# Kernel optimization log

Measured on AMD Instinct MI355X. Metric: run time of the kernel, lower is better.

Reference implementation:

```python
import jax, jax.numpy as jnp
import numpy as np

B, N, D = 8, 2048, 1024
DC = 1024          # d_center
K = 4              # num_centers
NUM_JUMPS = 2
SPAN = 2
FIN = (2 + 2 * NUM_JUMPS + 1) * D  # 7*D

def _gelu(x):
    return jax.nn.gelu(x, approximate=False)  # torch nn.GELU default is exact erf

def setup_inputs() -> dict:
    key = jax.random.key(0)
    ks = jax.random.split(key, 16)
    s = lambda k, *sh: jax.random.normal(k, sh, dtype=jnp.float32) * 0.02
    return {
        "queries": jax.random.normal(ks[0], (B, N, D), dtype=jnp.float32),
        "fr_w1": s(ks[1], FIN, D), "fr_b1": jnp.zeros((D,), jnp.float32),
        "fr_w2": s(ks[2], D, D),   "fr_b2": jnp.zeros((D,), jnp.float32),
        "tc_w1": s(ks[3], D, DC),  "tc_b1": jnp.zeros((DC,), jnp.float32),
        "tc_w2": s(ks[4], DC, DC), "tc_b2": jnp.zeros((DC,), jnp.float32),
        "centers": jax.random.normal(ks[5], (K, DC), dtype=jnp.float32),
        "fc_w1": s(ks[6], D + DC, D), "fc_b1": jnp.zeros((D,), jnp.float32),
        "fc_w2": s(ks[7], D, D),      "fc_b2": jnp.zeros((D,), jnp.float32),
        "g_w": s(ks[8], D + DC, D),   "g_b": jnp.zeros((D,), jnp.float32),
    }

def reference(queries, fr_w1, fr_b1, fr_w2, fr_b2,
              tc_w1, tc_b1, tc_w2, tc_b2, centers,
              fc_w1, fc_b1, fc_w2, fc_b2, g_w, g_b):
    x = queries
    shifts = [1, -1, 0]  # left, right, x
    for i in range(1, NUM_JUMPS + 1):
        shifts += [i * SPAN, -i * SPAN]
    fusion = jnp.concatenate([jnp.roll(x, s, axis=1) for s in shifts], axis=-1)  # [B,N,7D]
    x_ring = _gelu(fusion @ fr_w1 + fr_b1) @ fr_w2 + fr_b2                       # [B,N,D]
    token_proj = _gelu(x_ring @ tc_w1 + tc_b1) @ tc_w2 + tc_b2                   # [B,N,DC]
    w = jax.nn.softmax(jnp.einsum('bnd,kd->bnk', token_proj, centers), axis=-1)  # [B,N,K]
    weighted = jnp.einsum('bnk,kd->bnd', w, centers)                             # [B,N,DC]
    fus2 = jnp.concatenate([x_ring, weighted], axis=-1)                          # [B,N,D+DC]
    gate = jax.nn.sigmoid(fus2 @ g_w + g_b)
    fc = _gelu(fus2 @ fc_w1 + fc_b1) @ fc_w2 + fc_b2
    return gate * fc + (1.0 - gate) * x_ring
```

## Files before the change

kernel.cpp:

```cpp
#include <hip/hip_runtime.h>
#include <hip/hip_bf16.h>
#include <math.h>

typedef unsigned short u16;
typedef __attribute__((ext_vector_type(8))) short short8;
typedef __attribute__((ext_vector_type(4))) float f32x4;


__device__ __forceinline__ float bf2f(u16 b) {
  return __uint_as_float(((unsigned int)b) << 16);
}
__device__ __forceinline__ u16 f2bf(float f) {
  unsigned int u = __float_as_uint(f);
  u += 0x7FFFu + ((u >> 16) & 1u);
  return (u16)(u >> 16);
}
__device__ __forceinline__ float gelu_exact(float x) {
  return 0.5f * x * (1.0f + erff(x * 0.70710678118654752f));
}

__device__ __forceinline__ void cp16(const void* g, void* l) {
  __builtin_amdgcn_global_load_lds(
      (const __attribute__((address_space(1))) unsigned int*)g,
      (__attribute__((address_space(3))) unsigned int*)l, 16, 0, 0);
}

template <int MODE, bool GATHER>
__global__ __launch_bounds__(256) void gemm128(
    const u16* __restrict__ A, int lda, const u16* __restrict__ Wt, int K,
    const float* __restrict__ bias, const float* __restrict__ bias2,
    void* __restrict__ out0, int ldo0, void* __restrict__ out1,
    const float* __restrict__ gate, const float* __restrict__ xring) {
  __shared__ __align__(16) u16 As[128 * 64];
  __shared__ __align__(16) u16 Bs[128 * 64];

  const int tid = threadIdx.x;
  const int lane = tid & 63;
  const int wave = tid >> 6;
  const int wm = wave >> 1;
  const int wn = wave & 1;

  const unsigned linear = blockIdx.y * gridDim.x + blockIdx.x;
  const unsigned xcd = linear & 7u;
  const unsigned pos = linear >> 3;
  const unsigned bx = pos % gridDim.x;
  const unsigned by = xcd * (gridDim.y >> 3) + pos / gridDim.x;
  const int m0 = by * 128;
  const int n0 = bx * 128;

  const int srow = lane >> 3;
  const int sq = lane & 7;
  const int sqs = sq ^ srow;

  f32x4 acc[4][4];
#pragma unroll
  for (int i = 0; i < 4; i++)
#pragma unroll
    for (int j = 0; j < 4; j++) acc[i][j] = (f32x4){0.f, 0.f, 0.f, 0.f};

  for (int k0 = 0; k0 < K; k0 += 64) {
#pragma unroll
    for (int i = 0; i < 4; i++) {
      const int rloc = wave * 32 + i * 8 + srow;
      long gofs;
      if (GATHER) {
        const int seg = k0 >> 10;
        int shift;
        switch (seg) {
          case 0: shift = 1; break;
          case 1: shift = -1; break;
          case 2: shift = 0; break;
          case 3: shift = 2; break;
          case 4: shift = -2; break;
          case 5: shift = 4; break;
          default: shift = -4; break;
        }
        const int m = m0 + rloc;
        const int b = m >> 11;
        const int nsrc = ((m & 2047) - shift) & 2047;
        gofs = (long)((b << 11) | nsrc) * 1024 + (k0 & 1023) + sqs * 8;
      } else {
        gofs = (long)(m0 + rloc) * lda + k0 + sqs * 8;
      }
      cp16(A + gofs, &As[(wave * 32 + i * 8) * 64]);
    }
#pragma unroll
    for (int i = 0; i < 4; i++) {
      const int rloc = wave * 32 + i * 8 + srow;
      const long gofs = (long)(n0 + rloc) * K + k0 + sqs * 8;
      cp16(Wt + gofs, &Bs[(wave * 32 + i * 8) * 64]);
    }
    __syncthreads();

    const int q4 = lane >> 4;
    const int r16 = lane & 15;
#pragma unroll
    for (int kk = 0; kk < 2; kk++) {
      short8 af[4], bf[4];
#pragma unroll
      for (int mi = 0; mi < 4; mi++) {
        const int row = wm * 64 + mi * 16 + r16;
        const int q = (kk * 4 + q4) ^ (row & 7);
        af[mi] = *(const short8*)&As[row * 64 + q * 8];
      }
#pragma unroll
      for (int ni = 0; ni < 4; ni++) {
        const int row = wn * 64 + ni * 16 + r16;
        const int q = (kk * 4 + q4) ^ (row & 7);
        bf[ni] = *(const short8*)&Bs[row * 64 + q * 8];
      }
#pragma unroll
      for (int mi = 0; mi < 4; mi++)
#pragma unroll
        for (int ni = 0; ni < 4; ni++)
          acc[mi][ni] = __builtin_amdgcn_mfma_f32_16x16x32_bf16(
              af[mi], bf[ni], acc[mi][ni], 0, 0, 0);
    }
    __syncthreads();
  }

  const int ccol = lane & 15;
  const int crow = (lane >> 4) * 4;
#pragma unroll
  for (int mi = 0; mi < 4; mi++) {
#pragma unroll
    for (int ni = 0; ni < 4; ni++) {
#pragma unroll
      for (int r = 0; r < 4; r++) {
        const int m = m0 + wm * 64 + mi * 16 + crow + r;
        const int n = n0 + wn * 64 + ni * 16 + ccol;
        if (MODE == 5) {
          if (n < 1024) {
            const float v = acc[mi][ni][r] + bias[n];
            ((float*)out0)[(long)m * 1024 + n] = 1.0f / (1.0f + expf(-v));
          } else {
            const float v = acc[mi][ni][r] + bias2[n - 1024];
            ((u16*)out1)[(long)m * 1024 + (n - 1024)] = f2bf(gelu_exact(v));
          }
        } else {
          const float v = acc[mi][ni][r] + bias[n];
          if (MODE == 0) {
            ((u16*)out0)[(long)m * ldo0 + n] = f2bf(gelu_exact(v));
          } else if (MODE == 1) {
            ((float*)out1)[(long)m * 1024 + n] = v;
            ((u16*)out0)[(long)m * ldo0 + n] = f2bf(v);
          } else if (MODE == 2) {
            ((u16*)out0)[(long)m * ldo0 + n] = f2bf(v);
          } else {
            const float g = gate[(long)m * 1024 + n];
            const float xr = xring[(long)m * 1024 + n];
            ((float*)out0)[(long)m * ldo0 + n] = g * v + (1.0f - g) * xr;
          }
        }
      }
    }
  }
}

__global__ __launch_bounds__(256) void cast_bf16(const float* __restrict__ in,
                                                 u16* __restrict__ out, int n4) {
  const long i = (long)blockIdx.x * 256 + threadIdx.x;
  if (i < n4) {
    const float4 v = ((const float4*)in)[i];
    ushort4 o;
    o.x = f2bf(v.x); o.y = f2bf(v.y); o.z = f2bf(v.z); o.w = f2bf(v.w);
    ((ushort4*)out)[i] = o;
  }
}

__global__ __launch_bounds__(256) void transp_bf16(const float* __restrict__ in,
                                                   u16* __restrict__ out, int K,
                                                   int N) {
  __shared__ float tile[32][33];
  const int tx = threadIdx.x & 31;
  const int ty = threadIdx.x >> 5;
  const long r0 = (long)blockIdx.y * 32;
  const long c0 = (long)blockIdx.x * 32;
#pragma unroll
  for (int r = 0; r < 4; r++)
    tile[ty + r * 8][tx] = in[(r0 + ty + r * 8) * N + c0 + tx];
  __syncthreads();
#pragma unroll
  for (int r = 0; r < 4; r++)
    out[(c0 + ty + r * 8) * K + r0 + tx] = f2bf(tile[tx][ty + r * 8]);
}

__global__ __launch_bounds__(256) void fold_S(const float* __restrict__ tc_w2,
                                              const float* __restrict__ tc_b2,
                                              const float* __restrict__ centers,
                                              float* __restrict__ S,
                                              float* __restrict__ bc) {
  const int wave = threadIdx.x >> 6, lane = threadIdx.x & 63;
  if (blockIdx.x < 256) {
    const int d = blockIdx.x * 4 + wave;
    const float* row = tc_w2 + (long)d * 1024;
    float s0 = 0.f, s1 = 0.f, s2 = 0.f, s3 = 0.f;
    for (int e = lane; e < 1024; e += 64) {
      const float w = row[e];
      s0 += w * centers[e];
      s1 += w * centers[1024 + e];
      s2 += w * centers[2048 + e];
      s3 += w * centers[3072 + e];
    }
#pragma unroll
    for (int off = 32; off > 0; off >>= 1) {
      s0 += __shfl_xor(s0, off);
      s1 += __shfl_xor(s1, off);
      s2 += __shfl_xor(s2, off);
      s3 += __shfl_xor(s3, off);
    }
    if (lane == 0) {
      S[d] = s0; S[1024 + d] = s1; S[2048 + d] = s2; S[3072 + d] = s3;
    }
  } else {
    const int k = wave;
    float s = 0.f;
    for (int e = lane; e < 1024; e += 64) s += tc_b2[e] * centers[k * 1024 + e];
#pragma unroll
    for (int off = 32; off > 0; off >>= 1) s += __shfl_xor(s, off);
    if (lane == 0) bc[k] = s;
  }
}

__global__ __launch_bounds__(256) void centers_kernel(
    const u16* __restrict__ h2, const float* __restrict__ S,
    const float* __restrict__ bc, const float* __restrict__ centers,
    u16* __restrict__ fus2) {
  const int lane = threadIdx.x & 63;
  const int wave = threadIdx.x >> 6;
  const long t = (long)blockIdx.x * 4 + wave;
  const u16* row = h2 + t * 1024;
  float d0 = 0.f, d1 = 0.f, d2 = 0.f, d3 = 0.f;
#pragma unroll
  for (int j = 0; j < 2; j++) {
    const int dbase = j * 512 + lane * 8;
    const short8 v = *(const short8*)(row + dbase);
#pragma unroll
    for (int e = 0; e < 8; e++) {
      const float x = bf2f((u16)v[e]);
      const int d = dbase + e;
      d0 += x * S[d];
      d1 += x * S[1024 + d];
      d2 += x * S[2048 + d];
      d3 += x * S[3072 + d];
    }
  }
#pragma unroll
  for (int off = 32; off > 0; off >>= 1) {
    d0 += __shfl_xor(d0, off);
    d1 += __shfl_xor(d1, off);
    d2 += __shfl_xor(d2, off);
    d3 += __shfl_xor(d3, off);
  }
  d0 += bc[0]; d1 += bc[1]; d2 += bc[2]; d3 += bc[3];
  const float mx = fmaxf(fmaxf(d0, d1), fmaxf(d2, d3));
  float e0 = expf(d0 - mx), e1 = expf(d1 - mx), e2 = expf(d2 - mx),
        e3 = expf(d3 - mx);
  const float inv = 1.0f / (e0 + e1 + e2 + e3);
  e0 *= inv; e1 *= inv; e2 *= inv; e3 *= inv;
#pragma unroll
  for (int j = 0; j < 2; j++) {
    const int dbase = j * 512 + lane * 8;
    short8 o;
#pragma unroll
    for (int e = 0; e < 8; e++) {
      const int d = dbase + e;
      const float wv = e0 * centers[d] + e1 * centers[1024 + d] +
                       e2 * centers[2048 + d] + e3 * centers[3072 + d];
      o[e] = (short)f2bf(wv);
    }
    *(short8*)(fus2 + t * 2048 + 1024 + dbase) = o;
  }
}

extern "C" void kernel_launch(void* const* d_in, const int* in_sizes, int n_in,
                              void* d_out, int out_size, void* d_ws,
                              size_t ws_size, hipStream_t stream) {
  const float* queries = (const float*)d_in[0];
  const float* fr_w1 = (const float*)d_in[1];
  const float* fr_b1 = (const float*)d_in[2];
  const float* fr_w2 = (const float*)d_in[3];
  const float* fr_b2 = (const float*)d_in[4];
  const float* tc_w1 = (const float*)d_in[5];
  const float* tc_b1 = (const float*)d_in[6];
  const float* tc_w2 = (const float*)d_in[7];
  const float* tc_b2 = (const float*)d_in[8];
  const float* centers = (const float*)d_in[9];
  const float* fc_w1 = (const float*)d_in[10];
  const float* fc_b1 = (const float*)d_in[11];
  const float* fc_w2 = (const float*)d_in[12];
  const float* fc_b2 = (const float*)d_in[13];
  const float* g_w = (const float*)d_in[14];
  const float* g_b = (const float*)d_in[15];

  char* ws = (char*)d_ws;
  u16* Wt1 = (u16*)ws; ws += (size_t)7168 * 1024 * 2;
  u16* Wt2 = (u16*)ws; ws += (size_t)1024 * 1024 * 2;
  u16* Wt3 = (u16*)ws; ws += (size_t)1024 * 1024 * 2;
  u16* Wt6 = (u16*)ws; ws += (size_t)1024 * 1024 * 2;
  u16* WtG = (u16*)ws; ws += (size_t)2048 * 2048 * 2;
  u16* Xb = (u16*)ws;  ws += (size_t)16384 * 1024 * 2;
  u16* h1 = (u16*)ws;  ws += (size_t)16384 * 1024 * 2;
  float* xring = (float*)ws; ws += (size_t)16384 * 1024 * 4;
  u16* fus2 = (u16*)ws; ws += (size_t)16384 * 2048 * 2;
  float* S = (float*)ws; ws += (size_t)4 * 1024 * 4;
  float* bc = (float*)ws; ws += 4 * 4;
  float* gate = (float*)d_out;
  float* out = (float*)d_out;

  cast_bf16<<<16384, 256, 0, stream>>>(queries, Xb, 16384 * 1024 / 4);
  transp_bf16<<<dim3(32, 224), 256, 0, stream>>>(fr_w1, Wt1, 7168, 1024);
  transp_bf16<<<dim3(32, 32), 256, 0, stream>>>(fr_w2, Wt2, 1024, 1024);
  transp_bf16<<<dim3(32, 32), 256, 0, stream>>>(tc_w1, Wt3, 1024, 1024);
  transp_bf16<<<dim3(32, 32), 256, 0, stream>>>(fc_w2, Wt6, 1024, 1024);
  transp_bf16<<<dim3(32, 64), 256, 0, stream>>>(g_w, WtG, 2048, 1024);
  transp_bf16<<<dim3(32, 64), 256, 0, stream>>>(fc_w1, WtG + (size_t)1024 * 2048,
                                                2048, 1024);
  fold_S<<<260, 256, 0, stream>>>(tc_w2, tc_b2, centers, S, bc);

  const dim3 grid(8, 128);
  gemm128<0, true><<<grid, 256, 0, stream>>>(Xb, 0, Wt1, 7168, fr_b1, nullptr,
                                             h1, 1024, nullptr, nullptr, nullptr);
  gemm128<1, false><<<grid, 256, 0, stream>>>(h1, 1024, Wt2, 1024, fr_b2,
                                              nullptr, fus2, 2048, xring,
                                              nullptr, nullptr);
  gemm128<0, false><<<grid, 256, 0, stream>>>(fus2, 2048, Wt3, 1024, tc_b1,
                                              nullptr, Xb, 1024, nullptr,
                                              nullptr, nullptr);
  centers_kernel<<<4096, 256, 0, stream>>>(Xb, S, bc, centers, fus2);
  gemm128<5, false><<<dim3(16, 128), 256, 0, stream>>>(
      fus2, 2048, WtG, 2048, g_b, fc_b1, gate, 1024, Xb, nullptr, nullptr);
  gemm128<4, false><<<grid, 256, 0, stream>>>(Xb, 1024, Wt6, 1024, fc_b2,
                                              nullptr, out, 1024, nullptr,
                                              gate, xring);
}
```

Baseline: 910.1 us.

## Double-buffer A tiles in LDS and load B fragments directly into registers

The GEMM kernel now keeps two LDS buffers for the A tile, so the next tile is prefetched while MFMAs run on the current one, and only one barrier remains per iteration. B (weight) fragments are no longer staged through LDS. Each wave reads its MFMA fragments straight from global memory into registers and prefetches the next k-step into a second register set. This hides load latency and halves LDS traffic. The cost is more VGPR pressure, and the weight fragments are read from global memory by both M-waves without cross-wave sharing, which duplicates global/L2 reads of B.

Result: slower. 1.380 ms (+51.6%).

```diff
diff --git a/kernel.cpp b/kernel.cpp
--- a/kernel.cpp
+++ b/kernel.cpp
@@ -31,8 +31,8 @@
     const float* __restrict__ bias, const float* __restrict__ bias2,
     void* __restrict__ out0, int ldo0, void* __restrict__ out1,
     const float* __restrict__ gate, const float* __restrict__ xring) {
-  __shared__ __align__(16) u16 As[128 * 64];
-  __shared__ __align__(16) u16 Bs[128 * 64];
+  __shared__ __align__(16) u16 As0[128 * 64];
+  __shared__ __align__(16) u16 As1[128 * 64];
 
   const int tid = threadIdx.x;
   const int lane = tid & 63;
@@ -52,13 +52,21 @@
   const int sq = lane & 7;
   const int sqs = sq ^ srow;
 
+  const int r16 = lane & 15;
+  const int q4 = lane >> 4;
+
+  const u16* bbase[4];
+#pragma unroll
+  for (int ni = 0; ni < 4; ni++)
+    bbase[ni] = Wt + (long)(n0 + wn * 64 + ni * 16 + r16) * K + q4 * 8;
+
   f32x4 acc[4][4];
 #pragma unroll
   for (int i = 0; i < 4; i++)
 #pragma unroll
     for (int j = 0; j < 4; j++) acc[i][j] = (f32x4){0.f, 0.f, 0.f, 0.f};
 
-  for (int k0 = 0; k0 < K; k0 += 64) {
+  auto stageA = [&](int k0, u16* buf) {
 #pragma unroll
     for (int i = 0; i < 4; i++) {
       const int rloc = wave * 32 + i * 8 + srow;
@@ -82,45 +90,55 @@
       } else {
         gofs = (long)(m0 + rloc) * lda + k0 + sqs * 8;
       }
-      cp16(A + gofs, &As[(wave * 32 + i * 8) * 64]);
-    }
-#pragma unroll
-    for (int i = 0; i < 4; i++) {
-      const int rloc = wave * 32 + i * 8 + srow;
-      const long gofs = (long)(n0 + rloc) * K + k0 + sqs * 8;
-      cp16(Wt + gofs, &Bs[(wave * 32 + i * 8) * 64]);
-    }
-    __syncthreads();
-
-    const int q4 = lane >> 4;
-    const int r16 = lane & 15;
+      cp16(A + gofs, &buf[(wave * 32 + i * 8) * 64]);
+    }
+  };
+  auto loadB = [&](int k0, short8* bf) {
+#pragma unroll
+    for (int ni = 0; ni < 4; ni++)
+#pragma unroll
+      for (int kk = 0; kk < 2; kk++)
+        bf[ni * 2 + kk] = *(const short8*)(bbase[ni] + k0 + kk * 32);
+  };
+
+  const int niter = K >> 6;
+  short8 bcur[8], bnxt[8];
+  stageA(0, As0);
+  loadB(0, bcur);
+  __syncthreads();
+
+  u16* rd = As0;
+  u16* wr = As1;
+#pragma unroll 2
+  for (int it = 0; it < niter; ++it) {
+    if (it + 1 < niter) {
+      loadB((it + 1) << 6, bnxt);
+      stageA((it + 1) << 6, wr);
+    }
 #pragma unroll
     for (int kk = 0; kk < 2; kk++) {
-      short8 af[4], bf[4];
+      short8 af[4];
+      const int q = (kk * 4 + q4) ^ (r16 & 7);
 #pragma unroll
       for (int mi = 0; mi < 4; mi++) {
         const int row = wm * 64 + mi * 16 + r16;
-        const int q = (kk * 4 + q4) ^ (row & 7);
-        af[mi] = *(const short8*)&As[row * 64 + q * 8];
-      }
-#pragma unroll
-      for (int ni = 0; ni < 4; ni++) {
-        const int row = wn * 64 + ni * 16 + r16;
-        const int q = (kk * 4 + q4) ^ (row & 7);
-        bf[ni] = *(const short8*)&Bs[row * 64 + q * 8];
+        af[mi] = *(const short8*)&rd[row * 64 + q * 8];
       }
 #pragma unroll
       for (int mi = 0; mi < 4; mi++)
 #pragma unroll
         for (int ni = 0; ni < 4; ni++)
           acc[mi][ni] = __builtin_amdgcn_mfma_f32_16x16x32_bf16(
-              af[mi], bf[ni], acc[mi][ni], 0, 0, 0);
+              af[mi], bcur[ni * 2 + kk], acc[mi][ni], 0, 0, 0);
     }
     __syncthreads();
-  }
-
-  const int ccol = lane & 15;
-  const int crow = (lane >> 4) * 4;
+    u16* t = rd; rd = wr; wr = t;
+#pragma unroll
+    for (int j = 0; j < 8; j++) bcur[j] = bnxt[j];
+  }
+
+  const int ccol = r16;
+  const int crow = q4 * 4;
 #pragma unroll
   for (int mi = 0; mi < 4; mi++) {
 #pragma unroll
```

## Fold linear layers and center mixing algebraically to shrink GEMM chain

Applied to the files above, without the earlier changes.

Precomputes the composite weight fr_w2·tc_w1 so x_ring and the tc pre-activation come from one wider GEMM over h1 instead of two chained GEMMs. It also folds the weighted-centers half of the fus2 input into rank-4 corrections: per-token softmax weights are multiplied by precomputed centers×(g_w, fc_w1) bottom halves, so the gate/fc GEMM uses K=1024 instead of 2048. The centers kernel now writes only four softmax weights per token instead of a 1024-wide bf16 row. The cost is extra setup kernels (a weight-product GEMM and folds) and a changed rounding path, because the composite weight is rounded to bf16 and the tc input skips bf16 rounding of x_ring.

New measurement: 880.7 us. 3.2% less time.

```diff
diff --git a/kernel.cpp b/kernel.cpp
--- a/kernel.cpp
+++ b/kernel.cpp
@@ -30,7 +30,8 @@
     const u16* __restrict__ A, int lda, const u16* __restrict__ Wt, int K,
     const float* __restrict__ bias, const float* __restrict__ bias2,
     void* __restrict__ out0, int ldo0, void* __restrict__ out1,
-    const float* __restrict__ gate, const float* __restrict__ xring) {
+    void* __restrict__ out2, const float* __restrict__ p0,
+    const float* __restrict__ p1, const float* __restrict__ p2) {
   __shared__ __align__(16) u16 As[128 * 64];
   __shared__ __align__(16) u16 Bs[128 * 64];
 
@@ -124,32 +125,44 @@
 #pragma unroll
   for (int mi = 0; mi < 4; mi++) {
 #pragma unroll
-    for (int ni = 0; ni < 4; ni++) {
-#pragma unroll
-      for (int r = 0; r < 4; r++) {
-        const int m = m0 + wm * 64 + mi * 16 + crow + r;
+    for (int r = 0; r < 4; r++) {
+      const int m = m0 + wm * 64 + mi * 16 + crow + r;
+      float4 wrow;
+      if (MODE == 8) wrow = *(const float4*)(p0 + (size_t)m * 4);
+#pragma unroll
+      for (int ni = 0; ni < 4; ni++) {
         const int n = n0 + wn * 64 + ni * 16 + ccol;
-        if (MODE == 5) {
+        const float v = acc[mi][ni][r];
+        if (MODE == 0) {
+          ((u16*)out0)[(long)m * ldo0 + n] = f2bf(gelu_exact(v + bias[n]));
+        } else if (MODE == 4) {
+          const float g = p0[(long)m * 1024 + n];
+          const float xr = p1[(long)m * 1024 + n];
+          ((float*)out0)[(long)m * ldo0 + n] =
+              g * (v + bias[n]) + (1.0f - g) * xr;
+        } else if (MODE == 6) {
+          ((u16*)out0)[(long)m * ldo0 + n] = f2bf(v);
+        } else if (MODE == 7) {
           if (n < 1024) {
-            const float v = acc[mi][ni][r] + bias[n];
-            ((float*)out0)[(long)m * 1024 + n] = 1.0f / (1.0f + expf(-v));
+            const float s = v + bias[n];
+            ((float*)out1)[(long)m * 1024 + n] = s;
+            ((u16*)out0)[(long)m * 1024 + n] = f2bf(s);
           } else {
-            const float v = acc[mi][ni][r] + bias2[n - 1024];
-            ((u16*)out1)[(long)m * 1024 + (n - 1024)] = f2bf(gelu_exact(v));
+            const int nn = n - 1024;
+            ((u16*)out2)[(long)m * 1024 + nn] = f2bf(gelu_exact(v + bias2[nn]));
           }
-        } else {
-          const float v = acc[mi][ni][r] + bias[n];
-          if (MODE == 0) {
-            ((u16*)out0)[(long)m * ldo0 + n] = f2bf(gelu_exact(v));
-          } else if (MODE == 1) {
-            ((float*)out1)[(long)m * 1024 + n] = v;
-            ((u16*)out0)[(long)m * ldo0 + n] = f2bf(v);
-          } else if (MODE == 2) {
-            ((u16*)out0)[(long)m * ldo0 + n] = f2bf(v);
+        } else if (MODE == 8) {
+          if (n < 1024) {
+            const float4 g2 = *(const float4*)(p1 + (size_t)n * 4);
+            const float s = v + bias[n] + wrow.x * g2.x + wrow.y * g2.y +
+                            wrow.z * g2.z + wrow.w * g2.w;
+            ((float*)out0)[(long)m * 1024 + n] = 1.0f / (1.0f + expf(-s));
           } else {
-            const float g = gate[(long)m * 1024 + n];
-            const float xr = xring[(long)m * 1024 + n];
-            ((float*)out0)[(long)m * ldo0 + n] = g * v + (1.0f - g) * xr;
+            const int nn = n - 1024;
+            const float4 f2 = *(const float4*)(p2 + (size_t)nn * 4);
+            const float s = v + bias2[nn] + wrow.x * f2.x + wrow.y * f2.y +
+                            wrow.z * f2.z + wrow.w * f2.w;
+            ((u16*)out1)[(long)m * 1024 + nn] = f2bf(gelu_exact(s));
           }
         }
       }
@@ -185,14 +198,63 @@
     out[(c0 + ty + r * 8) * K + r0 + tx] = f2bf(tile[tx][ty + r * 8]);
 }
 
-__global__ __launch_bounds__(256) void fold_S(const float* __restrict__ tc_w2,
-                                              const float* __restrict__ tc_b2,
-                                              const float* __restrict__ centers,
-                                              float* __restrict__ S,
-                                              float* __restrict__ bc) {
+__global__ __launch_bounds__(256) void fold_all(
+    const u16* __restrict__ GbT, const u16* __restrict__ FbT,
+    const u16* __restrict__ Wt3, const float* __restrict__ centers,
+    const float* __restrict__ fr_b2, const float* __restrict__ tc_b1,
+    const float* __restrict__ tc_w2, const float* __restrict__ tc_b2,
+    float* __restrict__ G2T, float* __restrict__ F2T, float* __restrict__ c2,
+    float* __restrict__ S, float* __restrict__ bc) {
+  const int b = blockIdx.x;
   const int wave = threadIdx.x >> 6, lane = threadIdx.x & 63;
-  if (blockIdx.x < 256) {
-    const int d = blockIdx.x * 4 + wave;
+  if (b < 256) {
+    const int n = b * 4 + wave;
+    float g[4] = {0.f, 0.f, 0.f, 0.f}, f[4] = {0.f, 0.f, 0.f, 0.f};
+#pragma unroll
+    for (int p = 0; p < 2; p++) {
+      const int base = p * 512 + lane * 8;
+      const short8 gv = *(const short8*)(GbT + (long)n * 1024 + base);
+      const short8 fv = *(const short8*)(FbT + (long)n * 1024 + base);
+#pragma unroll
+      for (int e = 0; e < 8; e++) {
+        const float ge = bf2f((u16)gv[e]), fe = bf2f((u16)fv[e]);
+#pragma unroll
+        for (int k = 0; k < 4; k++) {
+          const float c = centers[k * 1024 + base + e];
+          g[k] += ge * c;
+          f[k] += fe * c;
+        }
+      }
+    }
+#pragma unroll
+    for (int k = 0; k < 4; k++)
+#pragma unroll
+      for (int off = 32; off > 0; off >>= 1) {
+        g[k] += __shfl_xor(g[k], off);
+        f[k] += __shfl_xor(f[k], off);
+      }
+    if (lane == 0) {
+#pragma unroll
+      for (int k = 0; k < 4; k++) {
+        G2T[n * 4 + k] = g[k];
+        F2T[n * 4 + k] = f[k];
+      }
+    }
+  } else if (b < 512) {
+    const int j = (b - 256) * 4 + wave;
+    float s = 0.f;
+#pragma unroll
+    for (int p = 0; p < 2; p++) {
+      const int base = p * 512 + lane * 8;
+      const short8 wv = *(const short8*)(Wt3 + (long)j * 1024 + base);
+#pragma unroll
+      for (int e = 0; e < 8; e++) s += fr_b2[base + e] * bf2f((u16)wv[e]);
+    }
+#pragma unroll
+    for (int off = 32; off > 0; off >>= 1) s += __shfl_xor(s, off);
+    if (lane == 0) c2[j] = s + tc_b1[j];
+  } else if (b < 768) {
+    const int d = (b - 512) * 4 + wave;
     const float* row = tc_w2 + (long)d * 1024;
     float s0 = 0.f, s1 = 0.f, s2 = 0.f, s3 = 0.f;
     for (int e = lane; e < 1024; e += 64) {
@@ -224,8 +286,7 @@
 
 __global__ __launch_bounds__(256) void centers_kernel(
     const u16* __restrict__ h2, const float* __restrict__ S,
-    const float* __restrict__ bc, const float* __restrict__ centers,
-    u16* __restrict__ fus2) {
+    const float* __restrict__ bc, float* __restrict__ wtok) {
   const int lane = threadIdx.x & 63;
   const int wave = threadIdx.x >> 6;
   const long t = (long)blockIdx.x * 4 + wave;
@@ -252,24 +313,13 @@
     d2 += __shfl_xor(d2, off);
     d3 += __shfl_xor(d3, off);
   }
-  d0 += bc[0]; d1 += bc[1]; d2 += bc[2]; d3 += bc[3];
-  const float mx = fmaxf(fmaxf(d0, d1), fmaxf(d2, d3));
-  float e0 = expf(d0 - mx), e1 = expf(d1 - mx), e2 = expf(d2 - mx),
-        e3 = expf(d3 - mx);
-  const float inv = 1.0f / (e0 + e1 + e2 + e3);
-  e0 *= inv; e1 *= inv; e2 *= inv; e3 *= inv;
-#pragma unroll
-  for (int j = 0; j < 2; j++) {
-    const int dbase = j * 512 + lane * 8;
-    short8 o;
-#pragma unroll
-    for (int e = 0; e < 8; e++) {
-      const int d = dbase + e;
-      const float wv = e0 * centers[d] + e1 * centers[1024 + d] +
-                       e2 * centers[2048 + d] + e3 * centers[3072 + d];
-      o[e] = (short)f2bf(wv);
-    }
-    *(short8*)(fus2 + t * 2048 + 1024 + dbase) = o;
+  if (lane == 0) {
+    d0 += bc[0]; d1 += bc[1]; d2 += bc[2]; d3 += bc[3];
+    const float mx = fmaxf(fmaxf(d0, d1), fmaxf(d2, d3));
+    float e0 = expf(d0 - mx), e1 = expf(d1 - mx), e2 = expf(d2 - mx),
+          e3 = expf(d3 - mx);
+    const float inv = 1.0f / (e0 + e1 + e2 + e3);
+    *(float4*)(wtok + t * 4) = (float4){e0 * inv, e1 * inv, e2 * inv, e3 * inv};
   }
 }
 
@@ -295,42 +345,57 @@
 
   char* ws = (char*)d_ws;
   u16* Wt1 = (u16*)ws; ws += (size_t)7168 * 1024 * 2;
-  u16* Wt2 = (u16*)ws; ws += (size_t)1024 * 1024 * 2;
   u16* Wt3 = (u16*)ws; ws += (size_t)1024 * 1024 * 2;
   u16* Wt6 = (u16*)ws; ws += (size_t)1024 * 1024 * 2;
-  u16* WtG = (u16*)ws; ws += (size_t)2048 * 2048 * 2;
+  u16* WtJ = (u16*)ws; ws += (size_t)2048 * 1024 * 2;
+  u16* WtG2 = (u16*)ws; ws += (size_t)2048 * 1024 * 2;
+  u16* Fw2b = (u16*)ws; ws += (size_t)1024 * 1024 * 2;
+  u16* GbT = (u16*)ws; ws += (size_t)1024 * 1024 * 2;
+  u16* FbT = (u16*)ws; ws += (size_t)1024 * 1024 * 2;
   u16* Xb = (u16*)ws;  ws += (size_t)16384 * 1024 * 2;
   u16* h1 = (u16*)ws;  ws += (size_t)16384 * 1024 * 2;
+  u16* xrb = (u16*)ws; ws += (size_t)16384 * 1024 * 2;
   float* xring = (float*)ws; ws += (size_t)16384 * 1024 * 4;
-  u16* fus2 = (u16*)ws; ws += (size_t)16384 * 2048 * 2;
+  float* wtok = (float*)ws; ws += (size_t)16384 * 4 * 4;
   float* S = (float*)ws; ws += (size_t)4 * 1024 * 4;
-  float* bc = (float*)ws; ws += 4 * 4;
+  float* G2T = (float*)ws; ws += (size_t)1024 * 4 * 4;
+  float* F2T = (float*)ws; ws += (size_t)1024 * 4 * 4;
+  float* c2 = (float*)ws; ws += (size_t)1024 * 4;
+  float* bc = (float*)ws; ws += 16;
   float* gate = (float*)d_out;
   float* out = (float*)d_out;
 
   cast_bf16<<<16384, 256, 0, stream>>>(queries, Xb, 16384 * 1024 / 4);
+  cast_bf16<<<1024, 256, 0, stream>>>(fr_w2, Fw2b, 1024 * 1024 / 4);
   transp_bf16<<<dim3(32, 224), 256, 0, stream>>>(fr_w1, Wt1, 7168, 1024);
-  transp_bf16<<<dim3(32, 32), 256, 0, stream>>>(fr_w2, Wt2, 1024, 1024);
   transp_bf16<<<dim3(32, 32), 256, 0, stream>>>(tc_w1, Wt3, 1024, 1024);
   transp_bf16<<<dim3(32, 32), 256, 0, stream>>>(fc_w2, Wt6, 1024, 1024);
-  transp_bf16<<<dim3(32, 64), 256, 0, stream>>>(g_w, WtG, 2048, 1024);
-  transp_bf16<<<dim3(32, 64), 256, 0, stream>>>(fc_w1, WtG + (size_t)1024 * 2048,
-                                                2048, 1024);
-  fold_S<<<260, 256, 0, stream>>>(tc_w2, tc_b2, centers, S, bc);
-
-  const dim3 grid(8, 128);
-  gemm128<0, true><<<grid, 256, 0, stream>>>(Xb, 0, Wt1, 7168, fr_b1, nullptr,
-                                             h1, 1024, nullptr, nullptr, nullptr);
-  gemm128<1, false><<<grid, 256, 0, stream>>>(h1, 1024, Wt2, 1024, fr_b2,
-                                              nullptr, fus2, 2048, xring,
-                                              nullptr, nullptr);
-  gemm128<0, false><<<grid, 256, 0, stream>>>(fus2, 2048, Wt3, 1024, tc_b1,
-                                              nullptr, Xb, 1024, nullptr,
-                                              nullptr, nullptr);
-  centers_kernel<<<4096, 256, 0, stream>>>(Xb, S, bc, centers, fus2);
-  gemm128<5, false><<<dim3(16, 128), 256, 0, stream>>>(
-      fus2, 2048, WtG, 2048, g_b, fc_b1, gate, 1024, Xb, nullptr, nullptr);
-  gemm128<4, false><<<grid, 256, 0, stream>>>(Xb, 1024, Wt6, 1024, fc_b2,
-                                              nullptr, out, 1024, nullptr,
-                                              gate, xring);
-}
+  transp_bf16<<<dim3(32, 32), 256, 0, stream>>>(fr_w2, WtJ, 1024, 1024);
+  transp_bf16<<<dim3(32, 32), 256, 0, stream>>>(g_w, WtG2, 1024, 1024);
+  transp_bf16<<<dim3(32, 32), 256, 0, stream>>>(fc_w1,
+                                                WtG2 + (size_t)1024 * 1024,
+                                                1024, 1024);
+  transp_bf16<<<dim3(32, 32), 256, 0, stream>>>(g_w + (size_t)1024 * 1024, GbT,
+                                                1024, 1024);
+  transp_bf16<<<dim3(32, 32), 256, 0, stream>>>(fc_w1 + (size_t)1024 * 1024,
+                                                FbT, 1024, 1024);
+  fold_all<<<769, 256, 0, stream>>>(GbT, FbT, Wt3, centers, fr_b2, tc_b1,
+                                    tc_w2, tc_b2, G2T, F2T, c2, S, bc);
+  gemm128<6, false><<<dim3(8, 8), 256, 0, stream>>>(
+      Wt3, 1024, Fw2b, 1024, nullptr, nullptr, WtJ + (size_t)1024 * 1024, 1024,
+      nullptr, nullptr, nullptr, nullptr, nullptr);
+
+  gemm128<0, true><<<dim3(8, 128), 256, 0, stream>>>(
+      Xb, 0, Wt1, 7168, fr_b1, nullptr, h1, 1024, nullptr, nullptr, nullptr,
+      nullptr, nullptr);
+  gemm128<7, false><<<dim3(16, 128), 256, 0, stream>>>(
+      h1, 1024, WtJ, 1024, fr_b2, c2, xrb, 1024, xring, Xb, nullptr, nullptr,
+      nullptr);
+  centers_kernel<<<4096, 256, 0, stream>>>(Xb, S, bc, wtok);
+  gemm128<8, false><<<dim3(16, 128), 256, 0, stream>>>(
+      xrb, 1024, WtG2, 1024, g_b, fc_b1, gate, 1024, h1, nullptr, wtok, G2T,
+      F2T);
+  gemm128<4, false><<<dim3(8, 128), 256, 0, stream>>>(
+      h1, 1024, Wt6, 1024, fc_b2, nullptr, out, 1024, nullptr, nullptr, gate,
+      xring, nullptr);
+}
```
